# Kernel optimization log

Measured on AMD Instinct MI355X. Metric: run time of the kernel, lower is better.

## Reference

```python
import jax, jax.numpy as jnp
import numpy as np

T, B, F_, H, D, C = 16, 1024, 512, 128, 8, 100  # trees, batch, feat, hidden, depth, classes
L = 2 ** (D + 1)  # n_leaf = 512


def _routing_tables():
    # Static per-leaf routing: node index and branch side at each depth.
    # Derived from compute_mu's gather indices:
    #   node(d, l) = 2^d - 1 + l // 2^(D+1-d);  side(d, l) = (l // 2^(D-d)) % 2
    l = np.arange(L)
    node = np.stack([(2 ** d - 1) + l // (2 ** (D + 1 - d)) for d in range(D + 1)])  # [D+1, L]
    side = np.stack([(l // (2 ** (D - d))) % 2 for d in range(D + 1)])               # [D+1, L]
    return jnp.asarray(node, dtype=jnp.int32), jnp.asarray(side.astype(np.bool_))


def setup_inputs() -> dict:
    key = jax.random.key(0)
    ks = jax.random.split(key, 4)
    return {
        "feat": jax.random.normal(ks[0], (B, F_), jnp.float32),
        "W1": jax.random.normal(ks[1], (T, F_, H), jnp.float32) * 0.05,
        "b1": jnp.zeros((T, H), jnp.float32),
        "W2": jax.random.normal(ks[2], (T, H, L), jnp.float32) * 0.05,
        "b2": jnp.zeros((T, L), jnp.float32),
        "pi": jax.random.uniform(ks[3], (T, L, C), jnp.float32, -2.0, 2.0),
    }


def reference(feat, W1, b1, W2, b2, pi):
    node, side = _routing_tables()
    # Per-tree MLP head (dropout is identity in eval mode).
    h = jax.nn.relu(jnp.einsum('bf,tfh->tbh', feat, W1) + b1[:, None, :])        # [T,B,H]
    p = jax.nn.sigmoid(jnp.einsum('tbh,thl->tbl', h, W2) + b2[:, None, :])       # [T,B,L]
    # compute_mu: product of routing probs along each root->leaf path.
    sel = p[:, :, node]                          # [T,B,D+1,L] gather (static indices)
    route = jnp.where(side, 1.0 - sel, sel)      # left -> p, right -> 1-p
    mu = jnp.prod(route, axis=2)                 # [T,B,L]
    # compute_py_x: mean over leaves then mean over trees of mu @ softmax(pi).
    leaf_p = jax.nn.softmax(pi, axis=-1)         # [T,L,C]
    py_x = jnp.einsum('tbl,tlc->bc', mu, leaf_p) / (L * T)  # [B,C]
    return jnp.log(py_x)
```

## Files before the change

### kernel.cpp

```cpp
#include <hip/hip_runtime.h>
#include <hip/hip_bf16.h>
#include <math.h>

#define T_ 16
#define B_ 1024
#define F_ 512
#define H_ 128
#define D_ 8
#define C_ 100
#define L_ 512
#define CP_ 112

typedef __attribute__((ext_vector_type(8))) short bf16x8_t;
typedef __attribute__((ext_vector_type(4))) short bf16x4_t;
typedef __attribute__((ext_vector_type(4))) float f32x4_t;

__device__ inline ushort f2bf(float x) {
  __hip_bfloat16 b = __float2bfloat16(x);
  return *(ushort*)&b;
}
__device__ inline float bf2f(ushort u) {
  union { unsigned int i; float f; } v;
  v.i = ((unsigned int)u) << 16;
  return v.f;
}

__global__ __launch_bounds__(256) void k0_cvt(
    const float* __restrict__ X, ushort* __restrict__ Y) {
  int i = (blockIdx.x * 256 + threadIdx.x) * 8;
  float4 a = *(const float4*)(X + i);
  float4 b = *(const float4*)(X + i + 4);
  bf16x8_t o;
  o[0] = (short)f2bf(a.x); o[1] = (short)f2bf(a.y);
  o[2] = (short)f2bf(a.z); o[3] = (short)f2bf(a.w);
  o[4] = (short)f2bf(b.x); o[5] = (short)f2bf(b.y);
  o[6] = (short)f2bf(b.z); o[7] = (short)f2bf(b.w);
  *(bf16x8_t*)(Y + i) = o;
}

__global__ __launch_bounds__(256) void k0_transpose(
    const float* __restrict__ X, ushort* __restrict__ XT, int K, int N) {
  __shared__ float tile[32][33];
  const int k0 = blockIdx.x * 32, n0 = blockIdx.y * 32, s = blockIdx.z;
  const int c = threadIdx.x & 31, r0 = threadIdx.x >> 5;
  const float* Xs = X + (size_t)s * K * N;
  ushort* XTs = XT + (size_t)s * N * K;
#pragma unroll
  for (int j = 0; j < 4; ++j)
    tile[r0 + 8 * j][c] = Xs[(size_t)(k0 + r0 + 8 * j) * N + n0 + c];
  __syncthreads();
#pragma unroll
  for (int j = 0; j < 4; ++j)
    XTs[(size_t)(n0 + r0 + 8 * j) * K + k0 + c] = f2bf(tile[c][r0 + 8 * j]);
}

__global__ __launch_bounds__(256) void k1_mfma(
    const ushort* __restrict__ feat, const ushort* __restrict__ W1T,
    const float* __restrict__ b1, ushort* __restrict__ h_out) {
  __shared__ ushort a_s[32][72];
  __shared__ ushort b_s[128][72];
  const int t = blockIdx.y, b0 = blockIdx.x * 32, tid = threadIdx.x;
  const int w = tid >> 6, lane = tid & 63, quad = lane >> 4, n = lane & 15;

  f32x4_t acc[2][2];
#pragma unroll
  for (int i = 0; i < 2; ++i)
#pragma unroll
    for (int j = 0; j < 2; ++j) acc[i][j] = (f32x4_t){0.f, 0.f, 0.f, 0.f};

  for (int kc = 0; kc < 8; ++kc) {
    __syncthreads();
    {
      int row = tid >> 3, col8 = (tid & 7) * 8;
      *(bf16x8_t*)&a_s[row][col8] =
          *(const bf16x8_t*)(feat + (size_t)(b0 + row) * F_ + kc * 64 + col8);
    }
#pragma unroll
    for (int i = 0; i < 4; ++i) {
      int idx = i * 256 + tid;
      int row = idx >> 3, col8 = (idx & 7) * 8;
      *(bf16x8_t*)&b_s[row][col8] =
          *(const bf16x8_t*)(W1T + ((size_t)t * H_ + row) * F_ + kc * 64 + col8);
    }
    __syncthreads();
#pragma unroll
    for (int ks = 0; ks < 64; ks += 32) {
      bf16x8_t af[2], bf[2];
#pragma unroll
      for (int mt = 0; mt < 2; ++mt)
        af[mt] = *(const bf16x8_t*)&a_s[mt * 16 + n][ks + quad * 8];
#pragma unroll
      for (int nt = 0; nt < 2; ++nt)
        bf[nt] = *(const bf16x8_t*)&b_s[w * 32 + nt * 16 + n][ks + quad * 8];
#pragma unroll
      for (int mt = 0; mt < 2; ++mt)
#pragma unroll
        for (int nt = 0; nt < 2; ++nt)
          acc[mt][nt] = __builtin_amdgcn_mfma_f32_16x16x32_bf16(
              af[mt], bf[nt], acc[mt][nt], 0, 0, 0);
    }
  }
  float bias[2] = {b1[t * H_ + w * 32 + n], b1[t * H_ + w * 32 + 16 + n]};
#pragma unroll
  for (int mt = 0; mt < 2; ++mt)
#pragma unroll
    for (int nt = 0; nt < 2; ++nt)
#pragma unroll
      for (int r = 0; r < 4; ++r) {
        int row = b0 + mt * 16 + quad * 4 + r;
        int col = w * 32 + nt * 16 + n;
        float v = acc[mt][nt][r] + bias[nt];
        h_out[((size_t)t * B_ + row) * H_ + col] = f2bf(v > 0.f ? v : 0.f);
      }
}

__global__ __launch_bounds__(256) void k2_mfma(
    const ushort* __restrict__ h, const ushort* __restrict__ W2T,
    const float* __restrict__ b2, ushort* __restrict__ mu) {
  __shared__ ushort h_s[32][136];
  __shared__ ushort w_s[64][136];
  __shared__ ushort p_s[32][520];
  const int t = blockIdx.y, b0 = blockIdx.x * 32, tid = threadIdx.x;
  const int w = tid >> 6, lane = tid & 63, quad = lane >> 4, n = lane & 15;

#pragma unroll
  for (int i = 0; i < 2; ++i) {
    int idx = i * 256 + tid;
    int row = idx >> 4, col8 = (idx & 15) * 8;
    *(bf16x8_t*)&h_s[row][col8] =
        *(const bf16x8_t*)(h + ((size_t)t * B_ + b0 + row) * H_ + col8);
  }

  for (int nc = 0; nc < 8; ++nc) {
    __syncthreads();
#pragma unroll
    for (int i = 0; i < 4; ++i) {
      int idx = i * 256 + tid;
      int row = idx >> 4, col8 = (idx & 15) * 8;
      *(bf16x8_t*)&w_s[row][col8] =
          *(const bf16x8_t*)(W2T + ((size_t)t * L_ + nc * 64 + row) * H_ + col8);
    }
    __syncthreads();
    f32x4_t acc[2];
    acc[0] = (f32x4_t){0.f, 0.f, 0.f, 0.f};
    acc[1] = (f32x4_t){0.f, 0.f, 0.f, 0.f};
#pragma unroll
    for (int ks = 0; ks < 128; ks += 32) {
      bf16x8_t bfrag = *(const bf16x8_t*)&w_s[w * 16 + n][ks + quad * 8];
#pragma unroll
      for (int mt = 0; mt < 2; ++mt) {
        bf16x8_t afrag = *(const bf16x8_t*)&h_s[mt * 16 + n][ks + quad * 8];
        acc[mt] = __builtin_amdgcn_mfma_f32_16x16x32_bf16(afrag, bfrag,
                                                          acc[mt], 0, 0, 0);
      }
    }
    int l = nc * 64 + w * 16 + n;
    float bias = b2[t * L_ + l];
#pragma unroll
    for (int mt = 0; mt < 2; ++mt)
#pragma unroll
      for (int r = 0; r < 4; ++r) {
        float x = acc[mt][r] + bias;
        p_s[mt * 16 + quad * 4 + r][l] = f2bf(1.0f / (1.0f + __expf(-x)));
      }
  }
  __syncthreads();

#pragma unroll
  for (int pass = 0; pass < 4; ++pass) {
    int b = pass * 8 + (tid >> 5);
    int s = tid & 31;
    float P = 1.f;
#pragma unroll
    for (int d = 0; d < 5; ++d) {
      int nd = (1 << d) - 1 + (s >> (5 - d));
      int sd = (s >> (4 - d)) & 1;
      float pv = bf2f(p_s[b][nd]);
      P *= sd ? (1.f - pv) : pv;
    }
    float p5 = bf2f(p_s[b][31 + s]);
    float q5[2] = {P * p5, P * (1.f - p5)};
    float q6[4], q7[8];
#pragma unroll
    for (int j = 0; j < 2; ++j) {
      float pv = bf2f(p_s[b][63 + 2 * s + j]);
      q6[2 * j] = q5[j] * pv;
      q6[2 * j + 1] = q5[j] * (1.f - pv);
    }
#pragma unroll
    for (int u = 0; u < 4; ++u) {
      float pv = bf2f(p_s[b][127 + 4 * s + u]);
      q7[2 * u] = q6[u] * pv;
      q7[2 * u + 1] = q6[u] * (1.f - pv);
    }
    bf16x8_t o0, o1;
#pragma unroll
    for (int v = 0; v < 8; ++v) {
      float pv = bf2f(p_s[b][255 + 8 * s + v]);
      ushort e0 = f2bf(q7[v] * pv);
      ushort e1 = f2bf(q7[v] * (1.f - pv));
      if (v < 4) { o0[2 * v] = (short)e0; o0[2 * v + 1] = (short)e1; }
      else       { o1[2 * (v - 4)] = (short)e0; o1[2 * (v - 4) + 1] = (short)e1; }
    }
    ushort* dst = mu + ((size_t)t * B_ + b0 + b) * L_ + s * 16;
    *(bf16x8_t*)dst = o0;
    *(bf16x8_t*)(dst + 8) = o1;
  }
}

__global__ __launch_bounds__(256) void k4_softmax(
    const float* __restrict__ pi, ushort* __restrict__ lp) {
  int row  = blockIdx.x * 4 + (threadIdx.x >> 6);
  int lane = threadIdx.x & 63;
  const float* x = pi + (size_t)row * C_;
  float v0 = (lane < C_) ? x[lane] : -1e30f;
  float v1 = (lane + 64 < C_) ? x[lane + 64] : -1e30f;
  float m = fmaxf(v0, v1);
#pragma unroll
  for (int off = 32; off; off >>= 1) m = fmaxf(m, __shfl_xor(m, off, 64));
  float e0 = __expf(v0 - m);
  float e1 = (lane + 64 < C_) ? __expf(v1 - m) : 0.0f;
  float s = e0 + e1;
#pragma unroll
  for (int off = 32; off; off >>= 1) s += __shfl_xor(s, off, 64);
  float inv = 1.0f / s;
  size_t base = (size_t)row * CP_;
  if (lane < C_) lp[base + lane] = f2bf(e0 * inv);
  int c2 = lane + 64;
  if (c2 < CP_) lp[base + c2] = f2bf(c2 < C_ ? e1 * inv : 0.0f);
}

__global__ __launch_bounds__(256) void k5_mfma(
    const ushort* __restrict__ mu, const ushort* __restrict__ lp,
    float* __restrict__ part) {
  __shared__ ushort bT[CP_ * 68];
  const int t   = blockIdx.y;
  const int m0  = blockIdx.x * 64;
  const int tid = threadIdx.x;
  const int wave = tid >> 6, lane = tid & 63;
  const int quad = lane >> 4;
  const int n    = lane & 15;
  const int mrow = m0 + wave * 16 + n;

  f32x4_t acc[7];
#pragma unroll
  for (int i = 0; i < 7; ++i) acc[i] = (f32x4_t){0.f, 0.f, 0.f, 0.f};

  const ushort* muRow = mu + ((size_t)t * B_ + mrow) * L_;
  const ushort* lp_t  = lp + (size_t)t * L_ * CP_;

  for (int k0 = 0; k0 < L_; k0 += 64) {
    __syncthreads();
#pragma unroll
    for (int i = 0; i < 28; ++i) {
      int e  = i * 256 + tid;
      int kk = e / CP_;
      int c  = e - kk * CP_;
      bT[c * 68 + kk] = lp_t[(size_t)(k0 + kk) * CP_ + c];
    }
    __syncthreads();
#pragma unroll
    for (int ks = 0; ks < 64; ks += 32) {
      bf16x8_t afrag = *(const bf16x8_t*)(muRow + k0 + ks + quad * 8);
#pragma unroll
      for (int nt = 0; nt < 7; ++nt) {
        const ushort* bb = &bT[(nt * 16 + n) * 68 + ks + quad * 8];
        bf16x4_t lo = *(const bf16x4_t*)(bb);
        bf16x4_t hi = *(const bf16x4_t*)(bb + 4);
        bf16x8_t bfrag;
#pragma unroll
        for (int j = 0; j < 4; ++j) { bfrag[j] = lo[j]; bfrag[4 + j] = hi[j]; }
        acc[nt] = __builtin_amdgcn_mfma_f32_16x16x32_bf16(afrag, bfrag, acc[nt], 0, 0, 0);
      }
    }
  }
#pragma unroll
  for (int nt = 0; nt < 7; ++nt) {
    int c = nt * 16 + n;
    if (c < C_) {
#pragma unroll
      for (int r = 0; r < 4; ++r) {
        int m = m0 + wave * 16 + quad * 4 + r;
        part[((size_t)t * B_ + m) * C_ + c] = acc[nt][r];
      }
    }
  }
}

__global__ __launch_bounds__(256) void k6_log(
    const float* __restrict__ part, float* __restrict__ out) {
  int i = blockIdx.x * 256 + threadIdx.x;
  if (i < B_ * C_) {
    float s = 0.0f;
#pragma unroll
    for (int t = 0; t < T_; ++t) s += part[(size_t)t * B_ * C_ + i];
    out[i] = logf(s * (1.0f / (L_ * T_)));
  }
}

extern "C" void kernel_launch(void* const* d_in, const int* in_sizes, int n_in,
                              void* d_out, int out_size, void* d_ws,
                              size_t ws_size, hipStream_t stream) {
  const float* feat = (const float*)d_in[0];
  const float* W1   = (const float*)d_in[1];
  const float* b1   = (const float*)d_in[2];
  const float* W2   = (const float*)d_in[3];
  const float* b2   = (const float*)d_in[4];
  const float* pi   = (const float*)d_in[5];
  float* out = (float*)d_out;

  char* ws = (char*)d_ws;
  ushort* feat_bf  = (ushort*)(ws);
  ushort* W1T_buf  = (ushort*)(ws + ((size_t)1 << 20));
  ushort* W2T_buf  = (ushort*)(ws + ((size_t)3 << 20));
  ushort* h_buf    = (ushort*)(ws + ((size_t)5 << 20));
  ushort* mu_buf   = (ushort*)(ws + ((size_t)9 << 20));
  ushort* leaf_buf = (ushort*)(ws + ((size_t)25 << 20));
  float*  part_buf = (float*)(ws + ((size_t)27 << 20));

  k0_cvt<<<(B_ * F_) / (256 * 8), 256, 0, stream>>>(feat, feat_bf);
  k0_transpose<<<dim3(F_ / 32, H_ / 32, T_), 256, 0, stream>>>(W1, W1T_buf, F_, H_);
  k0_transpose<<<dim3(H_ / 32, L_ / 32, T_), 256, 0, stream>>>(W2, W2T_buf, H_, L_);
  k4_softmax<<<(T_ * L_) / 4, 256, 0, stream>>>(pi, leaf_buf);
  k1_mfma<<<dim3(B_ / 32, T_), 256, 0, stream>>>(feat_bf, W1T_buf, b1, h_buf);
  k2_mfma<<<dim3(B_ / 32, T_), 256, 0, stream>>>(h_buf, W2T_buf, b2, mu_buf);
  k5_mfma<<<dim3(B_ / 64, T_), 256, 0, stream>>>(mu_buf, leaf_buf, part_buf);
  k6_log<<<(B_ * C_ + 255) / 256, 256, 0, stream>>>(part_buf, out);
}
```

Measured before the change: 120.9 us.

## Merge prep kernels into one launch and fuse both MLP GEMMs via shared memory

The four preprocessing kernels (feat conversion, two weight transposes, leaf softmax) become a single launch that picks its role from the block index. The first-layer GEMM is fused into the second-layer/routing kernel, so the hidden activations stay in shared memory and never round-trip through global memory. Shared-memory buffers are aliased to keep the footprint in check. The trade-off is one larger kernel whose occupancy may be limited by its shared-memory use.

```diff
diff --git a/kernel.cpp b/kernel.cpp
--- a/kernel.cpp
+++ b/kernel.cpp
@@ -25,110 +25,135 @@
   return v.f;
 }
 
-__global__ __launch_bounds__(256) void k0_cvt(
-    const float* __restrict__ X, ushort* __restrict__ Y) {
-  int i = (blockIdx.x * 256 + threadIdx.x) * 8;
-  float4 a = *(const float4*)(X + i);
-  float4 b = *(const float4*)(X + i + 4);
-  bf16x8_t o;
-  o[0] = (short)f2bf(a.x); o[1] = (short)f2bf(a.y);
-  o[2] = (short)f2bf(a.z); o[3] = (short)f2bf(a.w);
-  o[4] = (short)f2bf(b.x); o[5] = (short)f2bf(b.y);
-  o[6] = (short)f2bf(b.z); o[7] = (short)f2bf(b.w);
-  *(bf16x8_t*)(Y + i) = o;
-}
-
-__global__ __launch_bounds__(256) void k0_transpose(
-    const float* __restrict__ X, ushort* __restrict__ XT, int K, int N) {
+__global__ __launch_bounds__(256) void k_prep(
+    const float* __restrict__ feat, const float* __restrict__ W1,
+    const float* __restrict__ W2, const float* __restrict__ pi,
+    ushort* __restrict__ feat_bf, ushort* __restrict__ W1T,
+    ushort* __restrict__ W2T, ushort* __restrict__ lp) {
   __shared__ float tile[32][33];
-  const int k0 = blockIdx.x * 32, n0 = blockIdx.y * 32, s = blockIdx.z;
-  const int c = threadIdx.x & 31, r0 = threadIdx.x >> 5;
-  const float* Xs = X + (size_t)s * K * N;
-  ushort* XTs = XT + (size_t)s * N * K;
-#pragma unroll
-  for (int j = 0; j < 4; ++j)
-    tile[r0 + 8 * j][c] = Xs[(size_t)(k0 + r0 + 8 * j) * N + n0 + c];
-  __syncthreads();
-#pragma unroll
-  for (int j = 0; j < 4; ++j)
-    XTs[(size_t)(n0 + r0 + 8 * j) * K + k0 + c] = f2bf(tile[c][r0 + 8 * j]);
-}
-
-__global__ __launch_bounds__(256) void k1_mfma(
+  const int bid = blockIdx.x, tid = threadIdx.x;
+
+  if (bid < 256) {
+    int i = (bid * 256 + tid) * 8;
+    float4 a = *(const float4*)(feat + i);
+    float4 b = *(const float4*)(feat + i + 4);
+    bf16x8_t o;
+    o[0] = (short)f2bf(a.x); o[1] = (short)f2bf(a.y);
+    o[2] = (short)f2bf(a.z); o[3] = (short)f2bf(a.w);
+    o[4] = (short)f2bf(b.x); o[5] = (short)f2bf(b.y);
+    o[6] = (short)f2bf(b.z); o[7] = (short)f2bf(b.w);
+    *(bf16x8_t*)(feat_bf + i) = o;
+    return;
+  }
+  if (bid < 2304) {
+    const float* X; ushort* XT; int K, N, kb, nb, s;
+    if (bid < 1280) {
+      int r = bid - 256;  kb = r & 15; nb = (r >> 4) & 3;  s = r >> 6;
+      X = W1; XT = W1T; K = F_; N = H_;
+    } else {
+      int r = bid - 1280; kb = r & 3;  nb = (r >> 2) & 15; s = r >> 6;
+      X = W2; XT = W2T; K = H_; N = L_;
+    }
+    const int k0 = kb * 32, n0 = nb * 32;
+    const int c = tid & 31, r0 = tid >> 5;
+    const float* Xs = X + (size_t)s * K * N;
+    ushort* XTs = XT + (size_t)s * N * K;
+#pragma unroll
+    for (int j = 0; j < 4; ++j)
+      tile[r0 + 8 * j][c] = Xs[(size_t)(k0 + r0 + 8 * j) * N + n0 + c];
+    __syncthreads();
+#pragma unroll
+    for (int j = 0; j < 4; ++j)
+      XTs[(size_t)(n0 + r0 + 8 * j) * K + k0 + c] = f2bf(tile[c][r0 + 8 * j]);
+    return;
+  }
+  {
+    int row  = (bid - 2304) * 4 + (tid >> 6);
+    int lane = tid & 63;
+    const float* x = pi + (size_t)row * C_;
+    float v0 = (lane < C_) ? x[lane] : -1e30f;
+    float v1 = (lane + 64 < C_) ? x[lane + 64] : -1e30f;
+    float m = fmaxf(v0, v1);
+#pragma unroll
+    for (int off = 32; off; off >>= 1) m = fmaxf(m, __shfl_xor(m, off, 64));
+    float e0 = __expf(v0 - m);
+    float e1 = (lane + 64 < C_) ? __expf(v1 - m) : 0.0f;
+    float sm = e0 + e1;
+#pragma unroll
+    for (int off = 32; off; off >>= 1) sm += __shfl_xor(sm, off, 64);
+    float inv = 1.0f / sm;
+    size_t base = (size_t)row * CP_;
+    if (lane < C_) lp[base + lane] = f2bf(e0 * inv);
+    int c2 = lane + 64;
+    if (c2 < CP_) lp[base + c2] = f2bf(c2 < C_ ? e1 * inv : 0.0f);
+  }
+}
+
+__global__ __launch_bounds__(256) void k12_mfma(
     const ushort* __restrict__ feat, const ushort* __restrict__ W1T,
-    const float* __restrict__ b1, ushort* __restrict__ h_out) {
-  __shared__ ushort a_s[32][72];
-  __shared__ ushort b_s[128][72];
+    const float* __restrict__ b1, const ushort* __restrict__ W2T,
+    const float* __restrict__ b2, ushort* __restrict__ mu) {
+  __shared__ ushort smem[29696];
+  ushort (*h_s)[136] = (ushort(*)[136])smem;
+  ushort (*a_s)[72]  = (ushort(*)[72])(smem + 4352);
+  ushort (*b_s)[72]  = (ushort(*)[72])(smem + 6656);
+  ushort (*w_s)[136] = (ushort(*)[136])(smem + 4352);
+  ushort (*p_s)[520] = (ushort(*)[520])(smem + 13056);
+
   const int t = blockIdx.y, b0 = blockIdx.x * 32, tid = threadIdx.x;
   const int w = tid >> 6, lane = tid & 63, quad = lane >> 4, n = lane & 15;
 
-  f32x4_t acc[2][2];
-#pragma unroll
-  for (int i = 0; i < 2; ++i)
-#pragma unroll
-    for (int j = 0; j < 2; ++j) acc[i][j] = (f32x4_t){0.f, 0.f, 0.f, 0.f};
-
-  for (int kc = 0; kc < 8; ++kc) {
-    __syncthreads();
-    {
-      int row = tid >> 3, col8 = (tid & 7) * 8;
-      *(bf16x8_t*)&a_s[row][col8] =
-          *(const bf16x8_t*)(feat + (size_t)(b0 + row) * F_ + kc * 64 + col8);
-    }
-#pragma unroll
-    for (int i = 0; i < 4; ++i) {
-      int idx = i * 256 + tid;
-      int row = idx >> 3, col8 = (idx & 7) * 8;
-      *(bf16x8_t*)&b_s[row][col8] =
-          *(const bf16x8_t*)(W1T + ((size_t)t * H_ + row) * F_ + kc * 64 + col8);
-    }
-    __syncthreads();
-#pragma unroll
-    for (int ks = 0; ks < 64; ks += 32) {
-      bf16x8_t af[2], bf[2];
-#pragma unroll
-      for (int mt = 0; mt < 2; ++mt)
-        af[mt] = *(const bf16x8_t*)&a_s[mt * 16 + n][ks + quad * 8];
+  {
+    f32x4_t acc[2][2];
+#pragma unroll
+    for (int i = 0; i < 2; ++i)
+#pragma unroll
+      for (int j = 0; j < 2; ++j) acc[i][j] = (f32x4_t){0.f, 0.f, 0.f, 0.f};
+
+    for (int kc = 0; kc < 8; ++kc) {
+      __syncthreads();
+      {
+        int row = tid >> 3, col8 = (tid & 7) * 8;
+        *(bf16x8_t*)&a_s[row][col8] =
+            *(const bf16x8_t*)(feat + (size_t)(b0 + row) * F_ + kc * 64 + col8);
+      }
+#pragma unroll
+      for (int i = 0; i < 4; ++i) {
+        int idx = i * 256 + tid;
+        int row = idx >> 3, col8 = (idx & 7) * 8;
+        *(bf16x8_t*)&b_s[row][col8] =
+            *(const bf16x8_t*)(W1T + ((size_t)t * H_ + row) * F_ + kc * 64 + col8);
+      }
+      __syncthreads();
+#pragma unroll
+      for (int ks = 0; ks < 64; ks += 32) {
+        bf16x8_t af[2], bfr[2];
+#pragma unroll
+        for (int mt = 0; mt < 2; ++mt)
+          af[mt] = *(const bf16x8_t*)&a_s[mt * 16 + n][ks + quad * 8];
+#pragma unroll
+        for (int nt = 0; nt < 2; ++nt)
+          bfr[nt] = *(const bf16x8_t*)&b_s[w * 32 + nt * 16 + n][ks + quad * 8];
+#pragma unroll
+        for (int mt = 0; mt < 2; ++mt)
+#pragma unroll
+          for (int nt = 0; nt < 2; ++nt)
+            acc[mt][nt] = __builtin_amdgcn_mfma_f32_16x16x32_bf16(
+                af[mt], bfr[nt], acc[mt][nt], 0, 0, 0);
+      }
+    }
+    float bias[2] = {b1[t * H_ + w * 32 + n], b1[t * H_ + w * 32 + 16 + n]};
+#pragma unroll
+    for (int mt = 0; mt < 2; ++mt)
 #pragma unroll
       for (int nt = 0; nt < 2; ++nt)
-        bf[nt] = *(const bf16x8_t*)&b_s[w * 32 + nt * 16 + n][ks + quad * 8];
-#pragma unroll
-      for (int mt = 0; mt < 2; ++mt)
-#pragma unroll
-        for (int nt = 0; nt < 2; ++nt)
-          acc[mt][nt] = __builtin_amdgcn_mfma_f32_16x16x32_bf16(
-              af[mt], bf[nt], acc[mt][nt], 0, 0, 0);
-    }
-  }
-  float bias[2] = {b1[t * H_ + w * 32 + n], b1[t * H_ + w * 32 + 16 + n]};
-#pragma unroll
-  for (int mt = 0; mt < 2; ++mt)
-#pragma unroll
-    for (int nt = 0; nt < 2; ++nt)
-#pragma unroll
-      for (int r = 0; r < 4; ++r) {
-        int row = b0 + mt * 16 + quad * 4 + r;
-        int col = w * 32 + nt * 16 + n;
-        float v = acc[mt][nt][r] + bias[nt];
-        h_out[((size_t)t * B_ + row) * H_ + col] = f2bf(v > 0.f ? v : 0.f);
-      }
-}
-
-__global__ __launch_bounds__(256) void k2_mfma(
-    const ushort* __restrict__ h, const ushort* __restrict__ W2T,
-    const float* __restrict__ b2, ushort* __restrict__ mu) {
-  __shared__ ushort h_s[32][136];
-  __shared__ ushort w_s[64][136];
-  __shared__ ushort p_s[32][520];
-  const int t = blockIdx.y, b0 = blockIdx.x * 32, tid = threadIdx.x;
-  const int w = tid >> 6, lane = tid & 63, quad = lane >> 4, n = lane & 15;
-
-#pragma unroll
-  for (int i = 0; i < 2; ++i) {
-    int idx = i * 256 + tid;
-    int row = idx >> 4, col8 = (idx & 15) * 8;
-    *(bf16x8_t*)&h_s[row][col8] =
-        *(const bf16x8_t*)(h + ((size_t)t * B_ + b0 + row) * H_ + col8);
+#pragma unroll
+        for (int r = 0; r < 4; ++r) {
+          int row = mt * 16 + quad * 4 + r;
+          int col = w * 32 + nt * 16 + n;
+          float v = acc[mt][nt][r] + bias[nt];
+          h_s[row][col] = f2bf(v > 0.f ? v : 0.f);
+        }
   }
 
   for (int nc = 0; nc < 8; ++nc) {
@@ -206,28 +231,6 @@
     *(bf16x8_t*)dst = o0;
     *(bf16x8_t*)(dst + 8) = o1;
   }
-}
-
-__global__ __launch_bounds__(256) void k4_softmax(
-    const float* __restrict__ pi, ushort* __restrict__ lp) {
-  int row  = blockIdx.x * 4 + (threadIdx.x >> 6);
-  int lane = threadIdx.x & 63;
-  const float* x = pi + (size_t)row * C_;
-  float v0 = (lane < C_) ? x[lane] : -1e30f;
-  float v1 = (lane + 64 < C_) ? x[lane + 64] : -1e30f;
-  float m = fmaxf(v0, v1);
-#pragma unroll
-  for (int off = 32; off; off >>= 1) m = fmaxf(m, __shfl_xor(m, off, 64));
-  float e0 = __expf(v0 - m);
-  float e1 = (lane + 64 < C_) ? __expf(v1 - m) : 0.0f;
-  float s = e0 + e1;
-#pragma unroll
-  for (int off = 32; off; off >>= 1) s += __shfl_xor(s, off, 64);
-  float inv = 1.0f / s;
-  size_t base = (size_t)row * CP_;
-  if (lane < C_) lp[base + lane] = f2bf(e0 * inv);
-  int c2 = lane + 64;
-  if (c2 < CP_) lp[base + c2] = f2bf(c2 < C_ ? e1 * inv : 0.0f);
 }
 
 __global__ __launch_bounds__(256) void k5_mfma(
@@ -313,17 +316,14 @@
   ushort* feat_bf  = (ushort*)(ws);
   ushort* W1T_buf  = (ushort*)(ws + ((size_t)1 << 20));
   ushort* W2T_buf  = (ushort*)(ws + ((size_t)3 << 20));
-  ushort* h_buf    = (ushort*)(ws + ((size_t)5 << 20));
-  ushort* mu_buf   = (ushort*)(ws + ((size_t)9 << 20));
-  ushort* leaf_buf = (ushort*)(ws + ((size_t)25 << 20));
-  float*  part_buf = (float*)(ws + ((size_t)27 << 20));
-
-  k0_cvt<<<(B_ * F_) / (256 * 8), 256, 0, stream>>>(feat, feat_bf);
-  k0_transpose<<<dim3(F_ / 32, H_ / 32, T_), 256, 0, stream>>>(W1, W1T_buf, F_, H_);
-  k0_transpose<<<dim3(H_ / 32, L_ / 32, T_), 256, 0, stream>>>(W2, W2T_buf, H_, L_);
-  k4_softmax<<<(T_ * L_) / 4, 256, 0, stream>>>(pi, leaf_buf);
-  k1_mfma<<<dim3(B_ / 32, T_), 256, 0, stream>>>(feat_bf, W1T_buf, b1, h_buf);
-  k2_mfma<<<dim3(B_ / 32, T_), 256, 0, stream>>>(h_buf, W2T_buf, b2, mu_buf);
+  ushort* mu_buf   = (ushort*)(ws + ((size_t)5 << 20));
+  ushort* leaf_buf = (ushort*)(ws + ((size_t)21 << 20));
+  float*  part_buf = (float*)(ws + ((size_t)23 << 20));
+
+  k_prep<<<4352, 256, 0, stream>>>(feat, W1, W2, pi, feat_bf, W1T_buf,
+                                   W2T_buf, leaf_buf);
+  k12_mfma<<<dim3(B_ / 32, T_), 256, 0, stream>>>(feat_bf, W1T_buf, b1,
+                                                  W2T_buf, b2, mu_buf);
   k5_mfma<<<dim3(B_ / 64, T_), 256, 0, stream>>>(mu_buf, leaf_buf, part_buf);
   k6_log<<<(B_ * C_ + 255) / 256, 256, 0, stream>>>(part_buf, out);
 }
```

Result: faster. 114.5 us (-5.3%).
